# Performance work log

Measured on AMD Instinct MI355X. Metric: run time of the kernel, lower is better.

## Reference

```python
import jax, jax.numpy as jnp
from jax import lax
import numpy as np

B, N, NPOINT, NSAMPLE, C = 4, 8192, 2048, 32, 128
RADIUS = 0.2
H1, H2, OUT = 64, 128, 128  # mlp: (3+C)->H1->H2, sas: H2->OUT


def fps(xyz, npoint):
    # furthest point sampling: xyz (B,N,3) -> idx (B,npoint) int32
    b, n, _ = xyz.shape
    init_idx = jnp.zeros((b,), jnp.int32)

    def step(carry, _):
        dist, last = carry
        p = jnp.take_along_axis(xyz, last[:, None, None], axis=1)  # (B,1,3)
        d = jnp.sum((xyz - p) ** 2, axis=-1)                       # (B,N)
        dist = jnp.minimum(dist, d)
        nxt = jnp.argmax(dist, axis=-1).astype(jnp.int32)
        return (dist, nxt), nxt

    (_, _), rest = lax.scan(step, (jnp.full((b, n), 1e10, jnp.float32), init_idx),
                            None, length=npoint - 1)
    return jnp.concatenate([init_idx[None, :], rest], axis=0).T    # (B,npoint)


def ball_query(xyz, new_xyz, radius, nsample):
    # xyz (B,N,3), new_xyz (B,S,3) -> idx (B,S,nsample) int32
    n = xyz.shape[1]
    d2 = jnp.sum((new_xyz[:, :, None, :] - xyz[:, None, :, :]) ** 2, axis=-1)  # (B,S,N)
    ar = jnp.arange(n, dtype=jnp.int32)
    keys = jnp.where(d2 <= radius * radius, ar, n)  # valid -> own index, invalid -> N
    neg_vals, _ = lax.top_k(-keys, nsample)          # smallest nsample keys
    idx = -neg_vals
    first = idx[..., :1]
    return jnp.where(idx >= n, first, idx)           # pad invalid with first valid


def gather_points(pts, idx):
    # pts (B,N,D), idx (B,S,ns) -> (B,S,ns,D)
    b, s, ns = idx.shape
    flat = jnp.take_along_axis(pts, idx.reshape(b, s * ns, 1), axis=1)
    return flat.reshape(b, s, ns, -1)


def setup_inputs() -> dict:
    key = jax.random.key(0)
    ks = jax.random.split(key, 8)
    xyz = jax.random.uniform(ks[0], (B, N, 3), dtype=jnp.float32)
    features = jax.random.normal(ks[1], (B, C, N), dtype=jnp.float32)
    cin = C + 3
    W1 = jax.random.normal(ks[2], (H1, cin), dtype=jnp.float32) / np.sqrt(cin)
    b1 = jnp.zeros((H1,), jnp.float32)
    W2 = jax.random.normal(ks[3], (H2, H1), dtype=jnp.float32) / np.sqrt(H1)
    b2 = jnp.zeros((H2,), jnp.float32)
    Wsa = jax.random.normal(ks[4], (OUT, H2), dtype=jnp.float32) / np.sqrt(H2)
    bsa = jnp.zeros((OUT,), jnp.float32)
    return {"xyz": xyz, "features": features, "W1": W1, "b1": b1,
            "W2": W2, "b2": b2, "Wsa": Wsa, "bsa": bsa}


def reference(xyz, features, W1, b1, W2, b2, Wsa, bsa):
    center_idx = fps(xyz, NPOINT)                                   # (B,S)
    new_xyz = jnp.take_along_axis(xyz, center_idx[:, :, None], axis=1)  # (B,S,3)
    g_idx = ball_query(xyz, new_xyz, RADIUS, NSAMPLE)               # (B,S,ns)
    g_xyz = gather_points(xyz, g_idx) - new_xyz[:, :, None, :]      # (B,S,ns,3) relative coords
    g_feat = gather_points(features.transpose(0, 2, 1), g_idx)      # (B,S,ns,C)
    h = jnp.concatenate([g_xyz, g_feat], axis=-1)                   # (B,S,ns,3+C)
    h = jax.nn.relu(jnp.einsum('bsnc,oc->bsno', h, W1) + b1)        # shared 1x1-conv MLP
    h = jax.nn.relu(jnp.einsum('bsnc,oc->bsno', h, W2) + b2)
    pooled = jnp.max(h, axis=2)                                     # max over nsample -> (B,S,H2)
    out = jnp.einsum('bsc,oc->bso', pooled, Wsa) + bsa              # sas channel mixer
    return new_xyz, out.transpose(0, 2, 1)                          # (B,S,3), (B,OUT,S)
```

## Files before the change

### kernel.cpp

```cpp
#include <hip/hip_runtime.h>
#include <cstdint>
#include <cstddef>

#define NB 4
#define NN 8192
#define NPTS 2048
#define NSAMP 32
#define NC 128
#define CIN 131
#define NH1 64
#define NH2 128
#define NOUTC 128

typedef float v2f __attribute__((ext_vector_type(2)));

__device__ __forceinline__ float d2_exact(float ax, float ay, float az,
                                          float bx, float by, float bz) {
  float dx = ax - bx, dy = ay - by, dz = az - bz;
  return __fadd_rn(__fadd_rn(__fmul_rn(dx, dx), __fmul_rn(dy, dy)),
                   __fmul_rn(dz, dz));
}

#if __has_builtin(__builtin_amdgcn_mov_dpp)
template <int CTRL>
__device__ __forceinline__ float dppf(float v) {
  return __int_as_float(
      __builtin_amdgcn_mov_dpp(__float_as_int(v), CTRL, 0xF, 0xF, true));
}
template <int CTRL>
__device__ __forceinline__ int dppi(int v) {
  return __builtin_amdgcn_mov_dpp(v, CTRL, 0xF, 0xF, true);
}
#else
template <int CTRL>
__device__ __forceinline__ float dppf(float v) {
  const int m = (CTRL == 0xB1) ? 1 : (CTRL == 0x4E) ? 2 : (CTRL == 0x141) ? 7 : 15;
  return __shfl_xor(v, m);
}
template <int CTRL>
__device__ __forceinline__ int dppi(int v) {
  const int m = (CTRL == 0xB1) ? 1 : (CTRL == 0x4E) ? 2 : (CTRL == 0x141) ? 7 : 15;
  return __shfl_xor(v, m);
}
#endif

__device__ __forceinline__ void red_pair(float& bv, int& bi, float ov, int oi) {
  bool t = (ov > bv) || (ov == bv && oi < bi);
  bv = t ? ov : bv;
  bi = t ? oi : bi;
}

__global__ __launch_bounds__(1024, 1) void fps_kernel(
    const float* __restrict__ xyz, float* __restrict__ newxyz) {
#pragma clang fp contract(off)
  const int b = blockIdx.x;
  const int tid = threadIdx.x;
  const int lane = tid & 63;
  const int wid = tid >> 6;
  const float* xb = xyz + (size_t)b * NN * 3;

  v2f x2[4], y2[4], z2[4], dd[4];
#pragma unroll
  for (int p = 0; p < 4; ++p) {
    int j0 = tid + ((2 * p) << 10);
    int j1 = tid + ((2 * p + 1) << 10);
    x2[p].x = xb[j0 * 3 + 0]; x2[p].y = xb[j1 * 3 + 0];
    y2[p].x = xb[j0 * 3 + 1]; y2[p].y = xb[j1 * 3 + 1];
    z2[p].x = xb[j0 * 3 + 2]; z2[p].y = xb[j1 * 3 + 2];
    dd[p].x = 1e10f; dd[p].y = 1e10f;
  }

  __shared__ float vbuf[2][16];
  __shared__ int ibuf[2][16];
  __shared__ float cbuf[2][16][3];

  float cx = xb[0], cy = xb[1], cz = xb[2];
  if (tid == 0) {
    newxyz[(size_t)b * NPTS * 3 + 0] = cx;
    newxyz[(size_t)b * NPTS * 3 + 1] = cy;
    newxyz[(size_t)b * NPTS * 3 + 2] = cz;
  }

  for (int t = 1; t < NPTS; ++t) {
    const int par = t & 1;
    v2f pxv = {cx, cx}, pyv = {cy, cy}, pzv = {cz, cz};
    float bv = -1.0f;
    int bi = 0;
    float bwx = 0.f, bwy = 0.f, bwz = 0.f;
#pragma unroll
    for (int p = 0; p < 4; ++p) {
      v2f dx = x2[p] - pxv;
      v2f dy = y2[p] - pyv;
      v2f dz = z2[p] - pzv;
      v2f s = dx * dx + dy * dy + dz * dz;
      v2f nd;
      nd.x = fminf(dd[p].x, s.x);
      nd.y = fminf(dd[p].y, s.y);
      dd[p] = nd;
      {
        bool c = nd.x > bv;
        bv = c ? nd.x : bv; bi = c ? (tid + ((2 * p) << 10)) : bi;
        bwx = c ? x2[p].x : bwx; bwy = c ? y2[p].x : bwy; bwz = c ? z2[p].x : bwz;
      }
      {
        bool c = nd.y > bv;
        bv = c ? nd.y : bv; bi = c ? (tid + ((2 * p + 1) << 10)) : bi;
        bwx = c ? x2[p].y : bwx; bwy = c ? y2[p].y : bwy; bwz = c ? z2[p].y : bwz;
      }
    }
    red_pair(bv, bi, dppf<0xB1>(bv), dppi<0xB1>(bi));
    red_pair(bv, bi, dppf<0x4E>(bv), dppi<0x4E>(bi));
    red_pair(bv, bi, dppf<0x141>(bv), dppi<0x141>(bi));
    red_pair(bv, bi, dppf<0x140>(bv), dppi<0x140>(bi));
    red_pair(bv, bi, __shfl_xor(bv, 16), __shfl_xor(bi, 16));
    red_pair(bv, bi, __shfl_xor(bv, 32), __shfl_xor(bi, 32));
    if (tid == (bi & 1023)) {
      vbuf[par][wid] = bv;
      ibuf[par][wid] = bi;
      cbuf[par][wid][0] = bwx; cbuf[par][wid][1] = bwy; cbuf[par][wid][2] = bwz;
    }
    __syncthreads();
    float v2w = vbuf[par][lane & 15];
    int i2w = ibuf[par][lane & 15];
    red_pair(v2w, i2w, dppf<0xB1>(v2w), dppi<0xB1>(i2w));
    red_pair(v2w, i2w, dppf<0x4E>(v2w), dppi<0x4E>(i2w));
    red_pair(v2w, i2w, dppf<0x141>(v2w), dppi<0x141>(i2w));
    red_pair(v2w, i2w, dppf<0x140>(v2w), dppi<0x140>(i2w));
    const int slot = (i2w & 1023) >> 6;
    cx = cbuf[par][slot][0]; cy = cbuf[par][slot][1]; cz = cbuf[par][slot][2];
    if (tid == (i2w & 1023)) {
      size_t o = ((size_t)b * NPTS + t) * 3;
      newxyz[o + 0] = cx; newxyz[o + 1] = cy; newxyz[o + 2] = cz;
    }
  }
}

__global__ __launch_bounds__(256) void ballq_kernel(
    const float* __restrict__ xyz, const float* __restrict__ newxyz,
    int* __restrict__ bidx) {
  const int cid = blockIdx.x * 4 + (threadIdx.x >> 6);
  const int lane = threadIdx.x & 63;
  const int b = cid >> 11;
  const float* xb = xyz + (size_t)b * NN * 3;
  const float cx = newxyz[(size_t)cid * 3 + 0];
  const float cy = newxyz[(size_t)cid * 3 + 1];
  const float cz = newxyz[(size_t)cid * 3 + 2];
  int* ob = bidx + (size_t)cid * NSAMP;
  int total = 0;
  int first = -1;
  for (int c0 = 0; c0 < NN; c0 += 64) {
    int j = c0 + lane;
    float xx = xb[j * 3 + 0], yy = xb[j * 3 + 1], zz = xb[j * 3 + 2];
    float d2 = d2_exact(cx, cy, cz, xx, yy, zz);
    bool in = d2 <= 0.04f;
    unsigned long long m = __ballot(in);
    if (first < 0 && m) first = c0 + __builtin_ctzll(m);
    int pos = total + __popcll(m & ((1ull << lane) - 1ull));
    if (in && pos < NSAMP) ob[pos] = j;
    total += __popcll(m);
    if (total >= NSAMP) break;
  }
  if (total < NSAMP && lane < NSAMP - total) ob[total + lane] = first;
}

__global__ void tw_kernel(const float* __restrict__ W1, const float* __restrict__ W2,
                          const float* __restrict__ Wsa, float* __restrict__ w1t,
                          float* __restrict__ w2t, float* __restrict__ wsat) {
  int i = blockIdx.x * blockDim.x + threadIdx.x;
  if (i < CIN * NH1) w1t[i] = W1[(i % NH1) * CIN + (i / NH1)];
  if (i < NH1 * NH2) w2t[i] = W2[(i % NH2) * NH1 + (i / NH2)];
  if (i < NH2 * NOUTC) wsat[i] = Wsa[(i % NOUTC) * NH2 + (i / NOUTC)];
}

__global__ void tfeat_kernel(const float* __restrict__ feat, float* __restrict__ featT) {
  __shared__ float tile[32][33];
  const int b = blockIdx.z;
  const int n0 = blockIdx.x * 32, c0 = blockIdx.y * 32;
  const int tx = threadIdx.x, ty = threadIdx.y;
#pragma unroll
  for (int r = 0; r < 4; ++r)
    tile[ty + r * 8][tx] = feat[((size_t)b * NC + c0 + ty + r * 8) * NN + n0 + tx];
  __syncthreads();
#pragma unroll
  for (int r = 0; r < 4; ++r)
    featT[((size_t)b * NN + n0 + ty + r * 8) * NC + c0 + tx] = tile[tx][ty + r * 8];
}

#define HS 36
__global__ __launch_bounds__(256) void mlp_kernel(
    const float* __restrict__ xyz, const float* __restrict__ fsrc,
    const float* __restrict__ newxyz, const int* __restrict__ bidx,
    const float* __restrict__ w1t, const float* __restrict__ b1,
    const float* __restrict__ w2t, const float* __restrict__ b2,
    const float* __restrict__ wsat, const float* __restrict__ bsa,
    float* __restrict__ out1, int useT) {
  __shared__ float h[CIN * HS];
  __shared__ float h1[NH1 * HS];
  __shared__ float pl[256];
  __shared__ float pooled[NH2];
  __shared__ int sidx[NSAMP];
  __shared__ float sc[3];
  const int cid = blockIdx.x;
  const int b = cid >> 11;
  const int s = cid & 2047;
  const int tid = threadIdx.x;
  if (tid < NSAMP) sidx[tid] = bidx[(size_t)cid * NSAMP + tid];
  if (tid < 3) sc[tid] = newxyz[(size_t)cid * 3 + tid];
  __syncthreads();
  {
    const int ss = tid >> 3, q = tid & 7;
    const int j = sidx[ss];
    if (useT) {
      const float4* fr = (const float4*)(fsrc + ((size_t)b * NN + j) * NC + q * 16);
#pragma unroll
      for (int u = 0; u < 4; ++u) {
        float4 v = fr[u];
        int c = 3 + q * 16 + u * 4;
        h[(c + 0) * HS + ss] = v.x;
        h[(c + 1) * HS + ss] = v.y;
        h[(c + 2) * HS + ss] = v.z;
        h[(c + 3) * HS + ss] = v.w;
      }
    } else {
      for (int u = 0; u < 16; ++u) {
        int c = q * 16 + u;
        h[(3 + c) * HS + ss] = fsrc[((size_t)b * NC + c) * NN + j];
      }
    }
    if (q == 0) {
      const float* pr = xyz + ((size_t)b * NN + j) * 3;
      h[0 * HS + ss] = pr[0] - sc[0];
      h[1 * HS + ss] = pr[1] - sc[1];
      h[2 * HS + ss] = pr[2] - sc[2];
    }
  }
  __syncthreads();
  {
    const int o = tid & 63, sg = tid >> 6;
    float acc[8];
    const float bb = b1[o];
#pragma unroll
    for (int i = 0; i < 8; ++i) acc[i] = bb;
    const float4* hb = (const float4*)&h[sg * 8];
    for (int k = 0; k < CIN; ++k) {
      float w = w1t[k * NH1 + o];
      float4 a = hb[k * (HS / 4) + 0];
      float4 c = hb[k * (HS / 4) + 1];
      acc[0] = fmaf(w, a.x, acc[0]); acc[1] = fmaf(w, a.y, acc[1]);
      acc[2] = fmaf(w, a.z, acc[2]); acc[3] = fmaf(w, a.w, acc[3]);
      acc[4] = fmaf(w, c.x, acc[4]); acc[5] = fmaf(w, c.y, acc[5]);
      acc[6] = fmaf(w, c.z, acc[6]); acc[7] = fmaf(w, c.w, acc[7]);
    }
#pragma unroll
    for (int i = 0; i < 8; ++i) h1[o * HS + sg * 8 + i] = fmaxf(acc[i], 0.0f);
  }
  __syncthreads();
  {
    const int o = tid & 127, sg = tid >> 7;
    float acc[16];
    const float bb = b2[o];
#pragma unroll
    for (int i = 0; i < 16; ++i) acc[i] = bb;
    const float4* hb = (const float4*)&h1[sg * 16];
    for (int k = 0; k < NH1; ++k) {
      float w = w2t[k * NH2 + o];
#pragma unroll
      for (int u = 0; u < 4; ++u) {
        float4 a = hb[k * (HS / 4) + u];
        acc[u * 4 + 0] = fmaf(w, a.x, acc[u * 4 + 0]);
        acc[u * 4 + 1] = fmaf(w, a.y, acc[u * 4 + 1]);
        acc[u * 4 + 2] = fmaf(w, a.z, acc[u * 4 + 2]);
        acc[u * 4 + 3] = fmaf(w, a.w, acc[u * 4 + 3]);
      }
    }
    float pm = acc[0];
#pragma unroll
    for (int i = 1; i < 16; ++i) pm = fmaxf(pm, acc[i]);
    pl[sg * 128 + o] = pm;
  }
  __syncthreads();
  if (tid < NH2) pooled[tid] = fmaxf(fmaxf(pl[tid], pl[128 + tid]), 0.0f);
  __syncthreads();
  if (tid < NOUTC) {
    float acc = bsa[tid];
    for (int k = 0; k < NH2; ++k) acc = fmaf(pooled[k], wsat[k * NOUTC + tid], acc);
    out1[((size_t)b * NOUTC + tid) * NPTS + s] = acc;
  }
}

extern "C" void kernel_launch(void* const* d_in, const int* in_sizes, int n_in,
                              void* d_out, int out_size, void* d_ws, size_t ws_size,
                              hipStream_t stream) {
  const float* xyz = (const float*)d_in[0];
  const float* feat = (const float*)d_in[1];
  const float* W1 = (const float*)d_in[2];
  const float* b1 = (const float*)d_in[3];
  const float* W2 = (const float*)d_in[4];
  const float* b2 = (const float*)d_in[5];
  const float* Wsa = (const float*)d_in[6];
  const float* bsa = (const float*)d_in[7];
  float* out = (float*)d_out;
  float* newxyz = out;
  float* out1 = out + (size_t)NB * NPTS * 3;

  const size_t featT_f = (size_t)NB * NN * NC;
  const size_t small_f = (size_t)CIN * NH1 + NH1 * NH2 + NH2 * NOUTC +
                         (size_t)NB * NPTS * NSAMP;
  float* ws = (float*)d_ws;
  bool useT = ws_size >= (featT_f + small_f) * 4;
  float* featT = ws;
  float* w1t = ws + (useT ? featT_f : 0);
  float* w2t = w1t + CIN * NH1;
  float* wsat = w2t + NH1 * NH2;
  int* bidx = (int*)(wsat + NH2 * NOUTC);

  tw_kernel<<<64, 256, 0, stream>>>(W1, W2, Wsa, w1t, w2t, wsat);
  if (useT)
    tfeat_kernel<<<dim3(NN / 32, NC / 32, NB), dim3(32, 8), 0, stream>>>(feat, featT);
  fps_kernel<<<NB, 1024, 0, stream>>>(xyz, newxyz);
  ballq_kernel<<<NB * NPTS / 4, 256, 0, stream>>>(xyz, newxyz, bidx);
  mlp_kernel<<<NB * NPTS, 256, 0, stream>>>(xyz, useT ? featT : feat, newxyz, bidx,
                                            w1t, b1, w2t, b2, wsat, bsa, out1,
                                            (int)useT);
}
```

Measured before the change: 3.740 ms.

## Morton-sort points and skip far groups in furthest point sampling

Adds a sort kernel that buckets each batch's points into a 16^3 Morton-ordered grid, so each FPS thread holds 8 spatially nearby points per group. The FPS loop keeps a bounding sphere per group and skips the distance update when a lower bound shows the new center cannot lower that group's current max. It also halves block size to 512 and carries original indices to preserve tie-breaking. This trades an extra sort pass and workspace, plus per-thread branch divergence, for fewer distance evaluations in the serial FPS loop.

```diff
diff --git a/kernel.cpp b/kernel.cpp
--- a/kernel.cpp
+++ b/kernel.cpp
@@ -11,6 +11,7 @@
 #define NH1 64
 #define NH2 128
 #define NOUTC 128
+#define GCELLS 4096
 
 typedef float v2f __attribute__((ext_vector_type(2)));
 
@@ -49,8 +50,195 @@
   bv = t ? ov : bv;
   bi = t ? oi : bi;
 }
-
-__global__ __launch_bounds__(1024, 1) void fps_kernel(
+__device__ __forceinline__ void red3(float& bv, int& bi, int& bs,
+                                     float ov, int oi, int os) {
+  bool t = (ov > bv) || (ov == bv && oi < bi);
+  bv = t ? ov : bv;
+  bi = t ? oi : bi;
+  bs = t ? os : bs;
+}
+
+__device__ __forceinline__ int spread3(int v) {
+  return (v & 1) | ((v & 2) << 2) | ((v & 4) << 4) | ((v & 8) << 6);
+}
+
+__global__ __launch_bounds__(1024, 1) void sort_kernel(
+    const float* __restrict__ xyz, float* __restrict__ xs,
+    float* __restrict__ ys, float* __restrict__ zs, int* __restrict__ io) {
+  __shared__ int hist[GCELLS];
+  __shared__ int cbase[GCELLS];
+  __shared__ int wtot[16];
+  __shared__ int woff[16];
+  const int b = blockIdx.x;
+  const int tid = threadIdx.x;
+  const int lane = tid & 63;
+  const int wid = tid >> 6;
+  const float* xb = xyz + (size_t)b * NN * 3;
+  for (int i = tid; i < GCELLS; i += 1024) hist[i] = 0;
+  __syncthreads();
+  int cell[8];
+  float px[8], py[8], pz[8];
+#pragma unroll
+  for (int k = 0; k < 8; ++k) {
+    int j = tid + (k << 10);
+    float x = xb[j * 3 + 0], y = xb[j * 3 + 1], z = xb[j * 3 + 2];
+    px[k] = x; py[k] = y; pz[k] = z;
+    int cx = min(15, max(0, (int)(x * 16.0f)));
+    int cy = min(15, max(0, (int)(y * 16.0f)));
+    int cz = min(15, max(0, (int)(z * 16.0f)));
+    cell[k] = spread3(cx) | (spread3(cy) << 1) | (spread3(cz) << 2);
+    atomicAdd(&hist[cell[k]], 1);
+  }
+  __syncthreads();
+  const int i0 = tid * 4;
+  int h0 = hist[i0], h1 = hist[i0 + 1], h2 = hist[i0 + 2], h3 = hist[i0 + 3];
+  int s4 = h0 + h1 + h2 + h3;
+  int v = s4;
+#pragma unroll
+  for (int d = 1; d < 64; d <<= 1) {
+    int o = __shfl_up(v, d);
+    if (lane >= d) v += o;
+  }
+  if (lane == 63) wtot[wid] = v;
+  __syncthreads();
+  if (tid < 16) {
+    int acc = 0;
+    for (int w = 0; w < 16; ++w) {
+      if (w == tid) woff[tid] = acc;
+      acc += wtot[w];
+    }
+  }
+  __syncthreads();
+  int eb = woff[wid] + v - s4;
+  cbase[i0] = eb;
+  cbase[i0 + 1] = eb + h0;
+  cbase[i0 + 2] = eb + h0 + h1;
+  cbase[i0 + 3] = eb + h0 + h1 + h2;
+  __syncthreads();
+  for (int i = tid; i < GCELLS; i += 1024) hist[i] = 0;
+  __syncthreads();
+  const size_t bo = (size_t)b * NN;
+#pragma unroll
+  for (int k = 0; k < 8; ++k) {
+    int pos = cbase[cell[k]] + atomicAdd(&hist[cell[k]], 1);
+    xs[bo + pos] = px[k];
+    ys[bo + pos] = py[k];
+    zs[bo + pos] = pz[k];
+    io[bo + pos] = tid + (k << 10);
+  }
+}
+
+__global__ __launch_bounds__(512, 1) void fps_kernel(
+    const float* __restrict__ xyz, const float* __restrict__ xs,
+    const float* __restrict__ ys, const float* __restrict__ zs,
+    const int* __restrict__ io, float* __restrict__ newxyz) {
+#pragma clang fp contract(off)
+  const int b = blockIdx.x;
+  const int tid = threadIdx.x;
+  const int lane = tid & 63;
+  const int wid = tid >> 6;
+  const size_t bo = (size_t)b * NN;
+
+  float X[2][8], Y[2][8], Z[2][8], D[2][8];
+  int I[2][8];
+  float GCX[2], GCY[2], GCZ[2], GR[2];
+  float GV[2], GX[2], GY[2], GZ[2];
+  int GI[2];
+#pragma unroll
+  for (int p = 0; p < 2; ++p) {
+    float mx = 0.f, my = 0.f, mz = 0.f;
+#pragma unroll
+    for (int k = 0; k < 8; ++k) {
+      int s = p * 4096 + tid * 8 + k;
+      X[p][k] = xs[bo + s];
+      Y[p][k] = ys[bo + s];
+      Z[p][k] = zs[bo + s];
+      I[p][k] = io[bo + s];
+      D[p][k] = 1e10f;
+      mx += X[p][k]; my += Y[p][k]; mz += Z[p][k];
+    }
+    mx *= 0.125f; my *= 0.125f; mz *= 0.125f;
+    float r2m = 0.f;
+#pragma unroll
+    for (int k = 0; k < 8; ++k)
+      r2m = fmaxf(r2m, d2_exact(X[p][k], Y[p][k], Z[p][k], mx, my, mz));
+    GCX[p] = mx; GCY[p] = my; GCZ[p] = mz;
+    GR[p] = __fmul_rn(sqrtf(r2m), 1.0001f) + 1e-6f;
+    GV[p] = 1e10f;
+    GI[p] = I[p][0]; GX[p] = X[p][0]; GY[p] = Y[p][0]; GZ[p] = Z[p][0];
+  }
+
+  __shared__ float vbuf[2][8];
+  __shared__ int ibuf[2][8];
+  __shared__ float cbuf[2][8][3];
+
+  const float* xb = xyz + (size_t)b * NN * 3;
+  float cx = xb[0], cy = xb[1], cz = xb[2];
+  if (tid == 0) {
+    newxyz[(size_t)b * NPTS * 3 + 0] = cx;
+    newxyz[(size_t)b * NPTS * 3 + 1] = cy;
+    newxyz[(size_t)b * NPTS * 3 + 2] = cz;
+  }
+
+  for (int t = 1; t < NPTS; ++t) {
+    const int par = t & 1;
+#pragma unroll
+    for (int p = 0; p < 2; ++p) {
+      float d2c = d2_exact(GCX[p], GCY[p], GCZ[p], cx, cy, cz);
+      float lb = sqrtf(d2c) - GR[p];
+      float lbm = lb - 1e-3f;
+      bool skip = (lb > 2e-3f) && (__fmul_rn(lbm, lbm) >= GV[p]);
+      if (!skip) {
+        float gv = -1.f; int gi = 0;
+        float gx = 0.f, gy = 0.f, gz = 0.f;
+#pragma unroll
+        for (int k = 0; k < 8; ++k) {
+          float d2 = d2_exact(X[p][k], Y[p][k], Z[p][k], cx, cy, cz);
+          float nd = fminf(D[p][k], d2);
+          D[p][k] = nd;
+          bool c = (nd > gv) || (nd == gv && I[p][k] < gi);
+          gv = c ? nd : gv; gi = c ? I[p][k] : gi;
+          gx = c ? X[p][k] : gx; gy = c ? Y[p][k] : gy; gz = c ? Z[p][k] : gz;
+        }
+        GV[p] = gv; GI[p] = gi; GX[p] = gx; GY[p] = gy; GZ[p] = gz;
+      }
+    }
+    float bv = GV[0]; int bi = GI[0];
+    float bx = GX[0], by = GY[0], bz = GZ[0];
+    {
+      bool c = (GV[1] > bv) || (GV[1] == bv && GI[1] < bi);
+      bv = c ? GV[1] : bv; bi = c ? GI[1] : bi;
+      bx = c ? GX[1] : bx; by = c ? GY[1] : by; bz = c ? GZ[1] : bz;
+    }
+    float rv = bv; int ri = bi;
+    red_pair(rv, ri, dppf<0xB1>(rv), dppi<0xB1>(ri));
+    red_pair(rv, ri, dppf<0x4E>(rv), dppi<0x4E>(ri));
+    red_pair(rv, ri, dppf<0x141>(rv), dppi<0x141>(ri));
+    red_pair(rv, ri, dppf<0x140>(rv), dppi<0x140>(ri));
+    red_pair(rv, ri, __shfl_xor(rv, 16), __shfl_xor(ri, 16));
+    red_pair(rv, ri, __shfl_xor(rv, 32), __shfl_xor(ri, 32));
+    if (bi == ri) {
+      vbuf[par][wid] = rv;
+      ibuf[par][wid] = ri;
+      cbuf[par][wid][0] = bx; cbuf[par][wid][1] = by; cbuf[par][wid][2] = bz;
+    }
+    __syncthreads();
+    int sl = lane & 7;
+    float v2 = vbuf[par][sl];
+    int i2 = ibuf[par][sl];
+    int s2 = sl;
+    red3(v2, i2, s2, dppf<0xB1>(v2), dppi<0xB1>(i2), dppi<0xB1>(s2));
+    red3(v2, i2, s2, dppf<0x4E>(v2), dppi<0x4E>(i2), dppi<0x4E>(s2));
+    red3(v2, i2, s2, dppf<0x141>(v2), dppi<0x141>(i2), dppi<0x141>(s2));
+    cx = cbuf[par][s2][0]; cy = cbuf[par][s2][1]; cz = cbuf[par][s2][2];
+    if (bi == i2) {
+      size_t o = ((size_t)b * NPTS + t) * 3;
+      newxyz[o + 0] = bx; newxyz[o + 1] = by; newxyz[o + 2] = bz;
+    }
+  }
+}
+
+__global__ __launch_bounds__(1024, 1) void fps_nosort_kernel(
     const float* __restrict__ xyz, float* __restrict__ newxyz) {
 #pragma clang fp contract(off)
   const int b = blockIdx.x;
@@ -58,7 +246,6 @@
   const int lane = tid & 63;
   const int wid = tid >> 6;
   const float* xb = xyz + (size_t)b * NN * 3;
-
   v2f x2[4], y2[4], z2[4], dd[4];
 #pragma unroll
   for (int p = 0; p < 4; ++p) {
@@ -69,44 +256,35 @@
     z2[p].x = xb[j0 * 3 + 2]; z2[p].y = xb[j1 * 3 + 2];
     dd[p].x = 1e10f; dd[p].y = 1e10f;
   }
-
   __shared__ float vbuf[2][16];
   __shared__ int ibuf[2][16];
   __shared__ float cbuf[2][16][3];
-
   float cx = xb[0], cy = xb[1], cz = xb[2];
   if (tid == 0) {
     newxyz[(size_t)b * NPTS * 3 + 0] = cx;
     newxyz[(size_t)b * NPTS * 3 + 1] = cy;
     newxyz[(size_t)b * NPTS * 3 + 2] = cz;
   }
-
   for (int t = 1; t < NPTS; ++t) {
     const int par = t & 1;
-    v2f pxv = {cx, cx}, pyv = {cy, cy}, pzv = {cz, cz};
-    float bv = -1.0f;
-    int bi = 0;
+    float bv = -1.0f; int bi = 0;
     float bwx = 0.f, bwy = 0.f, bwz = 0.f;
 #pragma unroll
     for (int p = 0; p < 4; ++p) {
-      v2f dx = x2[p] - pxv;
-      v2f dy = y2[p] - pyv;
-      v2f dz = z2[p] - pzv;
+      v2f dx = x2[p] - (v2f){cx, cx};
+      v2f dy = y2[p] - (v2f){cy, cy};
+      v2f dz = z2[p] - (v2f){cz, cz};
       v2f s = dx * dx + dy * dy + dz * dz;
       v2f nd;
       nd.x = fminf(dd[p].x, s.x);
       nd.y = fminf(dd[p].y, s.y);
       dd[p] = nd;
-      {
-        bool c = nd.x > bv;
+      { bool c = nd.x > bv;
         bv = c ? nd.x : bv; bi = c ? (tid + ((2 * p) << 10)) : bi;
-        bwx = c ? x2[p].x : bwx; bwy = c ? y2[p].x : bwy; bwz = c ? z2[p].x : bwz;
-      }
-      {
-        bool c = nd.y > bv;
+        bwx = c ? x2[p].x : bwx; bwy = c ? y2[p].x : bwy; bwz = c ? z2[p].x : bwz; }
+      { bool c = nd.y > bv;
         bv = c ? nd.y : bv; bi = c ? (tid + ((2 * p + 1) << 10)) : bi;
-        bwx = c ? x2[p].y : bwx; bwy = c ? y2[p].y : bwy; bwz = c ? z2[p].y : bwz;
-      }
+        bwx = c ? x2[p].y : bwx; bwy = c ? y2[p].y : bwy; bwz = c ? z2[p].y : bwz; }
     }
     red_pair(bv, bi, dppf<0xB1>(bv), dppi<0xB1>(bi));
     red_pair(bv, bi, dppf<0x4E>(bv), dppi<0x4E>(bi));
@@ -115,8 +293,7 @@
     red_pair(bv, bi, __shfl_xor(bv, 16), __shfl_xor(bi, 16));
     red_pair(bv, bi, __shfl_xor(bv, 32), __shfl_xor(bi, 32));
     if (tid == (bi & 1023)) {
-      vbuf[par][wid] = bv;
-      ibuf[par][wid] = bi;
+      vbuf[par][wid] = bv; ibuf[par][wid] = bi;
       cbuf[par][wid][0] = bwx; cbuf[par][wid][1] = bwy; cbuf[par][wid][2] = bwz;
     }
     __syncthreads();
@@ -303,21 +480,35 @@
   float* newxyz = out;
   float* out1 = out + (size_t)NB * NPTS * 3;
 
-  const size_t featT_f = (size_t)NB * NN * NC;
+  const size_t sort_f = (size_t)NB * NN * 4;
   const size_t small_f = (size_t)CIN * NH1 + NH1 * NH2 + NH2 * NOUTC +
                          (size_t)NB * NPTS * NSAMP;
+  const size_t featT_f = (size_t)NB * NN * NC;
+
   float* ws = (float*)d_ws;
-  bool useT = ws_size >= (featT_f + small_f) * 4;
-  float* featT = ws;
-  float* w1t = ws + (useT ? featT_f : 0);
+  bool useSort = ws_size >= (sort_f + small_f) * 4;
+  bool useT = ws_size >= (sort_f + small_f + featT_f) * 4;
+
+  float* xs = ws;
+  float* ysr = xs + (size_t)NB * NN;
+  float* zsr = ysr + (size_t)NB * NN;
+  int* iosr = (int*)(zsr + (size_t)NB * NN);
+  float* base2 = useSort ? (ws + sort_f) : ws;
+  float* w1t = base2;
   float* w2t = w1t + CIN * NH1;
   float* wsat = w2t + NH1 * NH2;
   int* bidx = (int*)(wsat + NH2 * NOUTC);
+  float* featT = (float*)(bidx + (size_t)NB * NPTS * NSAMP);
 
   tw_kernel<<<64, 256, 0, stream>>>(W1, W2, Wsa, w1t, w2t, wsat);
   if (useT)
     tfeat_kernel<<<dim3(NN / 32, NC / 32, NB), dim3(32, 8), 0, stream>>>(feat, featT);
-  fps_kernel<<<NB, 1024, 0, stream>>>(xyz, newxyz);
+  if (useSort) {
+    sort_kernel<<<NB, 1024, 0, stream>>>(xyz, xs, ysr, zsr, iosr);
+    fps_kernel<<<NB, 512, 0, stream>>>(xyz, xs, ysr, zsr, iosr, newxyz);
+  } else {
+    fps_nosort_kernel<<<NB, 1024, 0, stream>>>(xyz, newxyz);
+  }
   ballq_kernel<<<NB * NPTS / 4, 256, 0, stream>>>(xyz, newxyz, bidx);
   mlp_kernel<<<NB * NPTS, 256, 0, stream>>>(xyz, useT ? featT : feat, newxyz, bidx,
                                             w1t, b1, w2t, b2, wsat, bsa, out1,
```

Measured after the change: 4.168 ms. 1.11x slower.
